# Optimization experiments

Hardware: AMD Instinct MI355X
Metric: run time of the kernel (lower is better)

Reference implementation:

```python
import jax, jax.numpy as jnp
import numpy as np

B_G = 16        # number of point clouds
N_PER = 32768   # points per cloud (equal -> no padding)
T = B_G * N_PER
CIN = 16
D = 32          # global_dim
H = 4           # num_heads
HD = D // H
L = 2           # layers
EPS_LN = 1e-5
EPS_Z = 1e-6


def setup_inputs() -> dict:
    key = jax.random.key(0)
    ks = jax.random.split(key, 32)
    r = lambda i, shape, s: (jax.random.normal(ks[i], shape, dtype=jnp.float32) * s)
    inp = {
        "x": r(0, (T, CIN), 1.0),
        "pos": r(1, (T, 3), 1.0),
        "batch": (jnp.arange(T, dtype=jnp.int32) // N_PER),
        "w_in": r(2, (CIN, D), CIN ** -0.5),
        "b_in": r(3, (D,), 0.02),
        "w_pos": r(4, (3, D), 3 ** -0.5),
        "b_pos": r(5, (D,), 0.02),
        "wq": r(6, (L, D, D), D ** -0.5),
        "bq": r(7, (L, D), 0.02),
        "wk": r(8, (L, D, D), D ** -0.5),
        "bk": r(9, (L, D), 0.02),
        "wv": r(10, (L, D, D), D ** -0.5),
        "bv": r(11, (L, D), 0.02),
        "wo": r(12, (L, D, D), D ** -0.5),
        "bo": r(13, (L, D), 0.02),
        "g1": jnp.ones((L, D), jnp.float32),
        "be1": jnp.zeros((L, D), jnp.float32),
        "w1": r(14, (L, D, 2 * D), D ** -0.5),
        "bf1": r(15, (L, 2 * D), 0.02),
        "w2": r(16, (L, 2 * D, D), (2 * D) ** -0.5),
        "bf2": r(17, (L, D), 0.02),
        "g2": jnp.ones((L, D), jnp.float32),
        "be2": jnp.zeros((L, D), jnp.float32),
    }
    return inp


def _layernorm(h, g, b):
    mu = jnp.mean(h, axis=-1, keepdims=True)
    var = jnp.mean(jnp.square(h - mu), axis=-1, keepdims=True)
    return (h - mu) * jax.lax.rsqrt(var + EPS_LN) * g + b


def _linear_attn(h, wq, bq, wk, bk, wv, bv, wo, bo):
    B, N, C = h.shape
    def heads(w, b):
        return (h @ w + b).reshape(B, N, H, HD).transpose(0, 2, 1, 3)  # [B,H,N,hd]
    q = jax.nn.elu(heads(wq, bq)) + 1.0   # ELU feature map phi(.)
    k = jax.nn.elu(heads(wk, bk)) + 1.0
    v = heads(wv, bv)
    kv = jnp.einsum("bhnd,bhne->bhde", k, v)            # O(N) KV summary
    ksum = k.sum(axis=2)                                   # [B,H,hd]
    z = 1.0 / (jnp.einsum("bhnd,bhd->bhn", q, ksum) + EPS_Z)
    out = jnp.einsum("bhnd,bhde->bhne", q, kv) * z[..., None]
    out = out.transpose(0, 2, 1, 3).reshape(B, N, C)
    return out @ wo + bo


def reference(x, pos, batch, w_in, b_in, w_pos, b_pos, wq, bq, wk, bk, wv, bv,
              wo, bo, g1, be1, w1, bf1, w2, bf2, g2, be2):
    # to_dense_batch: batch is sorted; compute per-point index within its segment
    counts = jax.ops.segment_sum(jnp.ones((T,), jnp.int32), batch, num_segments=B_G)
    starts = jnp.concatenate([jnp.zeros((1,), jnp.int32), jnp.cumsum(counts)[:-1]])
    idx = jnp.arange(T, dtype=jnp.int32) - starts[batch]
    x_dense = jnp.zeros((B_G, N_PER, CIN), x.dtype).at[batch, idx].set(x)
    pos_dense = jnp.zeros((B_G, N_PER, 3), pos.dtype).at[batch, idx].set(pos)

    h = (x_dense @ w_in + b_in) + (pos_dense @ w_pos + b_pos)  # [B,N,D]
    for l in range(L):
        h = _layernorm(h + _linear_attn(h, wq[l], bq[l], wk[l], bk[l],
                                        wv[l], bv[l], wo[l], bo[l]), g1[l], be1[l])
        ffn = jax.nn.relu(h @ w1[l] + bf1[l]) @ w2[l] + bf2[l]
        h = _layernorm(h + ffn, g2[l], be2[l])
    return h[batch, idx]  # back to [T, D] (h[mask])
```

## Files before the change

### kernel.cpp

```cpp
#include <hip/hip_runtime.h>

#define KVSZ 288
#define EPS_LN 1e-5f
#define EPS_Z  1e-6f

typedef __attribute__((ext_vector_type(8))) short bf16x8;
typedef __attribute__((ext_vector_type(4))) float f32x4;

#define MFMA(a, b, c) __builtin_amdgcn_mfma_f32_16x16x32_bf16(a, b, c, 0, 0, 0)

#define WQ  0
#define WO  1024
#define KVM 2048
#define W1  3072
#define W2  5120
#define WKN 7168
#define WVN 8192

__device__ __forceinline__ unsigned short f2bf(float f) {
  union { float f; unsigned u; } x; x.f = f;
  unsigned r = x.u + 0x7fff + ((x.u >> 16) & 1);
  return (unsigned short)(r >> 16);
}

__device__ __forceinline__ unsigned pkbf(float a, float b) {
#if __has_builtin(__builtin_amdgcn_cvt_pk_bf16_f32)
  typedef __attribute__((ext_vector_type(2))) __bf16 bf16x2_t;
  bf16x2_t v = __builtin_amdgcn_cvt_pk_bf16_f32(a, b);
  return __builtin_bit_cast(unsigned, v);
#else
  return (unsigned)f2bf(a) | ((unsigned)f2bf(b) << 16);
#endif
}

__device__ __forceinline__ void lds_fence() { asm volatile("s_waitcnt lgkmcnt(0)" ::: "memory"); }
__device__ __forceinline__ float phi(float x) { return x > 0.f ? x + 1.f : __expf(x); }

__device__ __forceinline__ int perm32(int kp) {
  return ((kp & 4) << 2) | (((kp >> 3) << 2) + (kp & 3));
}

__device__ __forceinline__ bf16x8 bbuild(f32x4 lo, f32x4 hi) {
  union { bf16x8 v; unsigned u[4]; } cv;
  cv.u[0] = pkbf(lo[0], lo[1]); cv.u[1] = pkbf(lo[2], lo[3]);
  cv.u[2] = pkbf(hi[0], hi[1]); cv.u[3] = pkbf(hi[2], hi[3]);
  return cv.v;
}

__device__ __forceinline__ void stage_a32(unsigned short* dst, const float* __restrict__ W,
                                          int N, int tid) {
  for (int i = tid; i < 32 * N; i += 256) {
    int n = i >> 5, kp = i & 31;
    dst[i] = f2bf(W[perm32(kp) * N + n]);
  }
}
__device__ __forceinline__ void stage_a64(unsigned short* dst, const float* __restrict__ W,
                                          int tid) {
  for (int i = tid; i < 64 * 32; i += 256) {
    int n = i >> 6, kp = i & 63;
    int kl = ((kp >> 5) << 5) + perm32(kp & 31);
    dst[i] = f2bf(W[kl * 32 + n]);
  }
}
__device__ __forceinline__ void stage_kvm_t(unsigned short* dst, const float* __restrict__ kvg,
                                            int tid) {
  for (int i = tid; i < 1024; i += 256) {
    int e = i >> 5, kp = i & 31;
    int d = perm32(kp);
    float v = ((d >> 3) == (e >> 3)) ? kvg[(e >> 3) * 64 + (d & 7) * 8 + (e & 7)] : 0.f;
    dst[i] = f2bf(v);
  }
}

__device__ __forceinline__ void ln_t(f32x4& a0, f32x4& a1, float4 g0, float4 g1,
                                     float4 b0, float4 b1) {
  float s = a0[0] + a0[1] + a0[2] + a0[3] + a1[0] + a1[1] + a1[2] + a1[3];
  s += __shfl_xor(s, 16); s += __shfl_xor(s, 32);
  float mu = s * (1.f / 32.f);
  float vv = 0.f;
#pragma unroll
  for (int r = 0; r < 4; r++) {
    a0[r] -= mu; a1[r] -= mu;
    vv += a0[r] * a0[r] + a1[r] * a1[r];
  }
  vv += __shfl_xor(vv, 16); vv += __shfl_xor(vv, 32);
  float rstd = rsqrtf(vv * (1.f / 32.f) + EPS_LN);
  a0[0] = a0[0] * rstd * g0.x + b0.x; a0[1] = a0[1] * rstd * g0.y + b0.y;
  a0[2] = a0[2] * rstd * g0.z + b0.z; a0[3] = a0[3] * rstd * g0.w + b0.w;
  a1[0] = a1[0] * rstd * g1.x + b1.x; a1[1] = a1[1] * rstd * g1.y + b1.y;
  a1[2] = a1[2] * rstd * g1.z + b1.z; a1[3] = a1[3] * rstd * g1.w + b1.w;
}

__device__ __forceinline__ void layer_core_t(
    f32x4* hc0, f32x4* hc1, const unsigned short* ws, int quad, int m,
    const float* __restrict__ bq, const float* __restrict__ bo,
    const float* __restrict__ g1, const float* __restrict__ be1,
    const float* __restrict__ bf1, const float* __restrict__ bf2,
    const float* __restrict__ g2, const float* __restrict__ be2,
    const float* __restrict__ kvg) {
  const int k0 = quad * 8, q4 = quad * 4;
  {
    const bf16x8 wqA0 = *(const bf16x8*)(ws + WQ + m * 32 + k0);
    const bf16x8 wqA1 = *(const bf16x8*)(ws + WQ + (16 + m) * 32 + k0);
    const bf16x8 kvA0 = *(const bf16x8*)(ws + KVM + m * 32 + k0);
    const bf16x8 kvA1 = *(const bf16x8*)(ws + KVM + (16 + m) * 32 + k0);
    const bf16x8 woA0 = *(const bf16x8*)(ws + WO + m * 32 + k0);
    const bf16x8 woA1 = *(const bf16x8*)(ws + WO + (16 + m) * 32 + k0);
    const float4 bq0 = *(const float4*)(bq + q4), bq1 = *(const float4*)(bq + 16 + q4);
    const float4 bo0 = *(const float4*)(bo + q4), bo1 = *(const float4*)(bo + 16 + q4);
    const float4 g10 = *(const float4*)(g1 + q4), g11 = *(const float4*)(g1 + 16 + q4);
    const float4 e10 = *(const float4*)(be1 + q4), e11 = *(const float4*)(be1 + 16 + q4);
    const float4 ks0 = *(const float4*)(kvg + 256 + q4);
    const float4 ks1 = *(const float4*)(kvg + 272 + q4);
#pragma unroll
    for (int mt = 0; mt < 4; mt++) {
      bf16x8 hB = bbuild(hc0[mt], hc1[mt]);
      f32x4 q0 = {bq0.x, bq0.y, bq0.z, bq0.w};
      f32x4 q1 = {bq1.x, bq1.y, bq1.z, bq1.w};
      q0 = MFMA(wqA0, hB, q0);
      q1 = MFMA(wqA1, hB, q1);
#pragma unroll
      for (int r = 0; r < 4; r++) { q0[r] = phi(q0[r]); q1[r] = phi(q1[r]); }
      bf16x8 qB = bbuild(q0, q1);
      f32x4 zz = {0.f, 0.f, 0.f, 0.f};
      f32x4 at0 = MFMA(kvA0, qB, zz);
      f32x4 at1 = MFMA(kvA1, qB, zz);
      float p0 = q0[0] * ks0.x + q0[1] * ks0.y + q0[2] * ks0.z + q0[3] * ks0.w;
      float p1 = q1[0] * ks1.x + q1[1] * ks1.y + q1[2] * ks1.z + q1[3] * ks1.w;
      p0 += __shfl_xor(p0, 16);
      p1 += __shfl_xor(p1, 16);
      float z0 = 1.f / (p0 + EPS_Z), z1 = 1.f / (p1 + EPS_Z);
      bf16x8 aB;
      {
        union { bf16x8 v; unsigned u[4]; } cv;
        cv.u[0] = pkbf(at0[0] * z0, at0[1] * z0); cv.u[1] = pkbf(at0[2] * z0, at0[3] * z0);
        cv.u[2] = pkbf(at1[0] * z1, at1[1] * z1); cv.u[3] = pkbf(at1[2] * z1, at1[3] * z1);
        aB = cv.v;
      }
      f32x4 h0 = hc0[mt], h1 = hc1[mt];
      h0[0] += bo0.x; h0[1] += bo0.y; h0[2] += bo0.z; h0[3] += bo0.w;
      h1[0] += bo1.x; h1[1] += bo1.y; h1[2] += bo1.z; h1[3] += bo1.w;
      h0 = MFMA(woA0, aB, h0);
      h1 = MFMA(woA1, aB, h1);
      ln_t(h0, h1, g10, g11, e10, e11);
      hc0[mt] = h0; hc1[mt] = h1;
    }
  }
  {
    bf16x8 w1A[4]; float4 b1f[4];
#pragma unroll
    for (int nt = 0; nt < 4; nt++) {
      w1A[nt] = *(const bf16x8*)(ws + W1 + (nt * 16 + m) * 32 + k0);
      b1f[nt] = *(const float4*)(bf1 + nt * 16 + q4);
    }
    const bf16x8 w2L0 = *(const bf16x8*)(ws + W2 + m * 64 + k0);
    const bf16x8 w2H0 = *(const bf16x8*)(ws + W2 + m * 64 + 32 + k0);
    const bf16x8 w2L1 = *(const bf16x8*)(ws + W2 + (16 + m) * 64 + k0);
    const bf16x8 w2H1 = *(const bf16x8*)(ws + W2 + (16 + m) * 64 + 32 + k0);
    const float4 b20 = *(const float4*)(bf2 + q4), b21 = *(const float4*)(bf2 + 16 + q4);
    const float4 g20 = *(const float4*)(g2 + q4), g21 = *(const float4*)(g2 + 16 + q4);
    const float4 e20 = *(const float4*)(be2 + q4), e21 = *(const float4*)(be2 + 16 + q4);
#pragma unroll
    for (int mt = 0; mt < 4; mt++) {
      bf16x8 hB = bbuild(hc0[mt], hc1[mt]);
      f32x4 hd[4];
#pragma unroll
      for (int nt = 0; nt < 4; nt++) {
        f32x4 ini = {b1f[nt].x, b1f[nt].y, b1f[nt].z, b1f[nt].w};
        hd[nt] = MFMA(w1A[nt], hB, ini);
#pragma unroll
        for (int r = 0; r < 4; r++) hd[nt][r] = fmaxf(hd[nt][r], 0.f);
      }
      bf16x8 fL = bbuild(hd[0], hd[1]);
      bf16x8 fH = bbuild(hd[2], hd[3]);
      f32x4 o0 = hc0[mt], o1 = hc1[mt];
      o0[0] += b20.x; o0[1] += b20.y; o0[2] += b20.z; o0[3] += b20.w;
      o1[0] += b21.x; o1[1] += b21.y; o1[2] += b21.z; o1[3] += b21.w;
      o0 = MFMA(w2L0, fL, o0);
      o0 = MFMA(w2H0, fH, o0);
      o1 = MFMA(w2L1, fL, o1);
      o1 = MFMA(w2H1, fH, o1);
      ln_t(o0, o1, g20, g21, e20, e21);
      hc0[mt] = o0; hc1[mt] = o1;
    }
  }
}

__device__ __forceinline__ void kv_stage_t(
    const f32x4* hc0, const f32x4* hc1, unsigned short* tw, const unsigned short* ws,
    int offk, int offv, float* blk, int quad, int m,
    const float* __restrict__ bk, const float* __restrict__ bv) {
  const int k0 = quad * 8, q4 = quad * 4;
  unsigned short* Tk = tw;
  unsigned short* Tv = tw + 1280;
  const bf16x8 wkA0 = *(const bf16x8*)(ws + offk + m * 32 + k0);
  const bf16x8 wkA1 = *(const bf16x8*)(ws + offk + (16 + m) * 32 + k0);
  const bf16x8 wvA0 = *(const bf16x8*)(ws + offv + m * 32 + k0);
  const bf16x8 wvA1 = *(const bf16x8*)(ws + offv + (16 + m) * 32 + k0);
  const float4 bk0 = *(const float4*)(bk + q4), bk1 = *(const float4*)(bk + 16 + q4);
  const float4 bv0 = *(const float4*)(bv + q4), bv1 = *(const float4*)(bv + 16 + q4);
  f32x4 accA = {0.f, 0.f, 0.f, 0.f}, accB = {0.f, 0.f, 0.f, 0.f};
  f32x4 ksa0 = {0.f, 0.f, 0.f, 0.f}, ksa1 = {0.f, 0.f, 0.f, 0.f};
#pragma unroll
  for (int ch = 0; ch < 2; ch++) {
#pragma unroll
    for (int mtl = 0; mtl < 2; mtl++) {
      int mt = ch * 2 + mtl;
      bf16x8 hB = bbuild(hc0[mt], hc1[mt]);
      f32x4 kn0 = {bk0.x, bk0.y, bk0.z, bk0.w};
      f32x4 kn1 = {bk1.x, bk1.y, bk1.z, bk1.w};
      f32x4 vn0 = {bv0.x, bv0.y, bv0.z, bv0.w};
      f32x4 vn1 = {bv1.x, bv1.y, bv1.z, bv1.w};
      kn0 = MFMA(wkA0, hB, kn0);
      kn1 = MFMA(wkA1, hB, kn1);
      vn0 = MFMA(wvA0, hB, vn0);
      vn1 = MFMA(wvA1, hB, vn1);
      int cb = mtl * 16 + m;
#pragma unroll
      for (int r = 0; r < 4; r++) {
        kn0[r] = phi(kn0[r]); kn1[r] = phi(kn1[r]);
        ksa0[r] += kn0[r];    ksa1[r] += kn1[r];
        Tk[(q4 + r) * 40 + cb]      = f2bf(kn0[r]);
        Tk[(16 + q4 + r) * 40 + cb] = f2bf(kn1[r]);
        Tv[(q4 + r) * 40 + cb]      = f2bf(vn0[r]);
        Tv[(16 + q4 + r) * 40 + cb] = f2bf(vn1[r]);
      }
    }
    lds_fence();
    bf16x8 akL = *(const bf16x8*)(Tk + m * 40 + k0);
    bf16x8 akH = *(const bf16x8*)(Tk + (16 + m) * 40 + k0);
    bf16x8 avL = *(const bf16x8*)(Tv + m * 40 + k0);
    bf16x8 avH = *(const bf16x8*)(Tv + (16 + m) * 40 + k0);
    accA = MFMA(akL, avL, accA);
    accB = MFMA(akH, avH, accB);
    lds_fence();
  }
#pragma unroll
  for (int r = 0; r < 4; r++) {
    float v0 = ksa0[r], v1 = ksa1[r];
    v0 += __shfl_xor(v0, 1); v0 += __shfl_xor(v0, 2); v0 += __shfl_xor(v0, 4); v0 += __shfl_xor(v0, 8);
    v1 += __shfl_xor(v1, 1); v1 += __shfl_xor(v1, 2); v1 += __shfl_xor(v1, 4); v1 += __shfl_xor(v1, 8);
    if (m == 0) {
      atomicAdd(&blk[256 + q4 + r], v0);
      atomicAdd(&blk[272 + q4 + r], v1);
    }
  }
  if ((quad >> 1) == (m >> 3)) {
    int h0 = quad >> 1, h1 = 2 + (quad >> 1), e = m & 7;
#pragma unroll
    for (int r = 0; r < 4; r++) {
      int d = (q4 + r) & 7;
      atomicAdd(&blk[h0 * 64 + d * 8 + e], accA[r]);
      atomicAdd(&blk[h1 * 64 + d * 8 + e], accB[r]);
    }
  }
}

__global__ __launch_bounds__(256) void k_embed(
    const float* __restrict__ x, const float* __restrict__ pos,
    const float* __restrict__ w_in, const float* __restrict__ b_in,
    const float* __restrict__ w_pos, const float* __restrict__ b_pos,
    const float* __restrict__ wk, const float* __restrict__ bk,
    const float* __restrict__ wv, const float* __restrict__ bv,
    float* __restrict__ hout, float* __restrict__ gkv) {
  __shared__ __align__(16) unsigned short ws[3072];
  __shared__ __align__(16) unsigned short tiles[4 * 2560];
  __shared__ float blk[KVSZ];
  const int tid = threadIdx.x;
  const int wv_ = tid >> 6, lane = tid & 63, quad = lane >> 4, m = lane & 15;
  unsigned short* tw = tiles + wv_ * 2560;
  for (int i = tid; i < 1024; i += 256) {
    int n = i >> 5, k = i & 31;
    float v = k < 16 ? w_in[k * 32 + n] : (k < 19 ? w_pos[(k - 16) * 32 + n] : 0.f);
    ws[i] = f2bf(v);
  }
  stage_a32(ws + 1024, wk, 32, tid);
  stage_a32(ws + 2048, wv, 32, tid);
  for (int i = tid; i < KVSZ; i += 256) blk[i] = 0.f;
  __syncthreads();
  const int wbase = blockIdx.x * 256 + wv_ * 64;
  const int cloud = blockIdx.x >> 7;
  const int k0 = quad * 8, q4 = quad * 4;
  const bf16x8 weA0 = *(const bf16x8*)(ws + m * 32 + k0);
  const bf16x8 weA1 = *(const bf16x8*)(ws + (16 + m) * 32 + k0);
  float4 bi0, bi1;
  {
    float4 a = *(const float4*)(b_in + q4), b = *(const float4*)(b_pos + q4);
    bi0 = make_float4(a.x + b.x, a.y + b.y, a.z + b.z, a.w + b.w);
    float4 c = *(const float4*)(b_in + 16 + q4), d = *(const float4*)(b_pos + 16 + q4);
    bi1 = make_float4(c.x + d.x, c.y + d.y, c.z + d.z, c.w + d.w);
  }
  f32x4 hc0[4], hc1[4];
#pragma unroll
  for (int mt = 0; mt < 4; mt++) {
    int p = wbase + mt * 16 + m;
    union { bf16x8 v; unsigned u[4]; } xb;
    xb.u[0] = xb.u[1] = xb.u[2] = xb.u[3] = 0;
    if (quad < 2) {
      const float4* xp = (const float4*)(x + (size_t)p * 16 + quad * 8);
      float4 t0 = xp[0], t1 = xp[1];
      xb.u[0] = pkbf(t0.x, t0.y); xb.u[1] = pkbf(t0.z, t0.w);
      xb.u[2] = pkbf(t1.x, t1.y); xb.u[3] = pkbf(t1.z, t1.w);
    } else if (quad == 2) {
      const float* pp = pos + (size_t)p * 3;
      xb.u[0] = pkbf(pp[0], pp[1]); xb.u[1] = pkbf(pp[2], 0.f);
    }
    f32x4 i0 = {bi0.x, bi0.y, bi0.z, bi0.w};
    f32x4 i1 = {bi1.x, bi1.y, bi1.z, bi1.w};
    hc0[mt] = MFMA(weA0, xb.v, i0);
    hc1[mt] = MFMA(weA1, xb.v, i1);
    float* hp = hout + (size_t)p * 32;
    *(float4*)(hp + q4)      = make_float4(hc0[mt][0], hc0[mt][1], hc0[mt][2], hc0[mt][3]);
    *(float4*)(hp + 16 + q4) = make_float4(hc1[mt][0], hc1[mt][1], hc1[mt][2], hc1[mt][3]);
  }
  kv_stage_t(hc0, hc1, tw, ws, 1024, 2048, blk, quad, m, bk, bv);
  __syncthreads();
  float* g = gkv + cloud * KVSZ;
  for (int i = tid; i < KVSZ; i += 256) atomicAdd(&g[i], blk[i]);
}

__global__ __launch_bounds__(256) void k_mid(
    const float* __restrict__ wq, const float* __restrict__ bq,
    const float* __restrict__ wo, const float* __restrict__ bo,
    const float* __restrict__ g1, const float* __restrict__ be1,
    const float* __restrict__ w1, const float* __restrict__ bf1,
    const float* __restrict__ w2, const float* __restrict__ bf2,
    const float* __restrict__ g2, const float* __restrict__ be2,
    const float* __restrict__ wkn, const float* __restrict__ bkn,
    const float* __restrict__ wvn, const float* __restrict__ bvn,
    const float* __restrict__ kv_in, float* __restrict__ gkv_out,
    float* __restrict__ hbuf) {
  __shared__ __align__(16) unsigned short ws[9216];
  __shared__ __align__(16) unsigned short tiles[4 * 2560];
  __shared__ float blk[KVSZ];
  const int tid = threadIdx.x;
  const int wv_ = tid >> 6, lane = tid & 63, quad = lane >> 4, m = lane & 15;
  unsigned short* tw = tiles + wv_ * 2560;
  const int cloud = blockIdx.x >> 7;
  stage_a32(ws + WQ, wq, 32, tid);
  stage_a32(ws + WO, wo, 32, tid);
  stage_kvm_t(ws + KVM, kv_in + cloud * KVSZ, tid);
  stage_a32(ws + W1, w1, 64, tid);
  stage_a64(ws + W2, w2, tid);
  stage_a32(ws + WKN, wkn, 32, tid);
  stage_a32(ws + WVN, wvn, 32, tid);
  for (int i = tid; i < KVSZ; i += 256) blk[i] = 0.f;
  __syncthreads();
  const int wbase = blockIdx.x * 256 + wv_ * 64;
  const int q4 = quad * 4;
  f32x4 hc0[4], hc1[4];
#pragma unroll
  for (int mt = 0; mt < 4; mt++) {
    const float* hp = hbuf + (size_t)(wbase + mt * 16 + m) * 32;
    float4 lo = *(const float4*)(hp + q4);
    float4 hi = *(const float4*)(hp + 16 + q4);
    hc0[mt][0] = lo.x; hc0[mt][1] = lo.y; hc0[mt][2] = lo.z; hc0[mt][3] = lo.w;
    hc1[mt][0] = hi.x; hc1[mt][1] = hi.y; hc1[mt][2] = hi.z; hc1[mt][3] = hi.w;
  }
  layer_core_t(hc0, hc1, ws, quad, m, bq, bo, g1, be1, bf1, bf2, g2, be2,
               kv_in + cloud * KVSZ);
#pragma unroll
  for (int mt = 0; mt < 4; mt++) {
    float* hp = hbuf + (size_t)(wbase + mt * 16 + m) * 32;
    *(float4*)(hp + q4)      = make_float4(hc0[mt][0], hc0[mt][1], hc0[mt][2], hc0[mt][3]);
    *(float4*)(hp + 16 + q4) = make_float4(hc1[mt][0], hc1[mt][1], hc1[mt][2], hc1[mt][3]);
  }
  kv_stage_t(hc0, hc1, tw, ws, WKN, WVN, blk, quad, m, bkn, bvn);
  __syncthreads();
  float* g = gkv_out + cloud * KVSZ;
  for (int i = tid; i < KVSZ; i += 256) atomicAdd(&g[i], blk[i]);
}

__global__ __launch_bounds__(256) void k_last(
    const float* __restrict__ wq, const float* __restrict__ bq,
    const float* __restrict__ wo, const float* __restrict__ bo,
    const float* __restrict__ g1, const float* __restrict__ be1,
    const float* __restrict__ w1, const float* __restrict__ bf1,
    const float* __restrict__ w2, const float* __restrict__ bf2,
    const float* __restrict__ g2, const float* __restrict__ be2,
    const float* __restrict__ kv_in, float* __restrict__ hbuf) {
  __shared__ __align__(16) unsigned short ws[7168];
  const int tid = threadIdx.x;
  const int wv_ = tid >> 6, lane = tid & 63, quad = lane >> 4, m = lane & 15;
  const int cloud = blockIdx.x >> 7;
  stage_a32(ws + WQ, wq, 32, tid);
  stage_a32(ws + WO, wo, 32, tid);
  stage_kvm_t(ws + KVM, kv_in + cloud * KVSZ, tid);
  stage_a32(ws + W1, w1, 64, tid);
  stage_a64(ws + W2, w2, tid);
  __syncthreads();
  const int wbase = blockIdx.x * 256 + wv_ * 64;
  const int q4 = quad * 4;
  f32x4 hc0[4], hc1[4];
#pragma unroll
  for (int mt = 0; mt < 4; mt++) {
    const float* hp = hbuf + (size_t)(wbase + mt * 16 + m) * 32;
    float4 lo = *(const float4*)(hp + q4);
    float4 hi = *(const float4*)(hp + 16 + q4);
    hc0[mt][0] = lo.x; hc0[mt][1] = lo.y; hc0[mt][2] = lo.z; hc0[mt][3] = lo.w;
    hc1[mt][0] = hi.x; hc1[mt][1] = hi.y; hc1[mt][2] = hi.z; hc1[mt][3] = hi.w;
  }
  layer_core_t(hc0, hc1, ws, quad, m, bq, bo, g1, be1, bf1, bf2, g2, be2,
               kv_in + cloud * KVSZ);
#pragma unroll
  for (int mt = 0; mt < 4; mt++) {
    float* hp = hbuf + (size_t)(wbase + mt * 16 + m) * 32;
    *(float4*)(hp + q4)      = make_float4(hc0[mt][0], hc0[mt][1], hc0[mt][2], hc0[mt][3]);
    *(float4*)(hp + 16 + q4) = make_float4(hc1[mt][0], hc1[mt][1], hc1[mt][2], hc1[mt][3]);
  }
}

extern "C" void kernel_launch(void* const* d_in, const int* in_sizes, int n_in,
                              void* d_out, int out_size, void* d_ws, size_t ws_size,
                              hipStream_t stream) {
  (void)in_sizes; (void)n_in; (void)out_size; (void)ws_size;
  const float* x     = (const float*)d_in[0];
  const float* pos   = (const float*)d_in[1];
  const float* w_in  = (const float*)d_in[3];
  const float* b_in  = (const float*)d_in[4];
  const float* w_pos = (const float*)d_in[5];
  const float* b_pos = (const float*)d_in[6];
  const float* wq  = (const float*)d_in[7];
  const float* bq  = (const float*)d_in[8];
  const float* wk  = (const float*)d_in[9];
  const float* bk  = (const float*)d_in[10];
  const float* wv  = (const float*)d_in[11];
  const float* bv  = (const float*)d_in[12];
  const float* wo  = (const float*)d_in[13];
  const float* bo  = (const float*)d_in[14];
  const float* g1  = (const float*)d_in[15];
  const float* be1 = (const float*)d_in[16];
  const float* w1  = (const float*)d_in[17];
  const float* bf1 = (const float*)d_in[18];
  const float* w2  = (const float*)d_in[19];
  const float* bf2 = (const float*)d_in[20];
  const float* g2  = (const float*)d_in[21];
  const float* be2 = (const float*)d_in[22];
  float* out   = (float*)d_out;
  float* kvbuf = (float*)d_ws;

  hipMemsetAsync(kvbuf, 0, 2 * 16 * KVSZ * sizeof(float), stream);
  dim3 grid(2048), block(256);
  k_embed<<<grid, block, 0, stream>>>(x, pos, w_in, b_in, w_pos, b_pos,
                                      wk, bk, wv, bv, out, kvbuf);
  k_mid<<<grid, block, 0, stream>>>(wq, bq, wo, bo, g1, be1, w1, bf1, w2, bf2, g2, be2,
                                    wk + 1024, bk + 32, wv + 1024, bv + 32,
                                    kvbuf, kvbuf + 16 * KVSZ, out);
  k_last<<<grid, block, 0, stream>>>(wq + 1024, bq + 32, wo + 1024, bo + 32,
                                     g1 + 32, be1 + 32, w1 + 2048, bf1 + 64,
                                     w2 + 2048, bf2 + 32, g2 + 32, be2 + 32,
                                     kvbuf + 16 * KVSZ, out);
}
```

Baseline: 306.9 us.

## Fuse three layer kernels into one persistent kernel with grid barriers

```diff
diff --git a/kernel.cpp b/kernel.cpp
--- a/kernel.cpp
+++ b/kernel.cpp
@@ -3,6 +3,7 @@
 #define KVSZ 288
 #define EPS_LN 1e-5f
 #define EPS_Z  1e-6f
+#define NBLK 512
 
 typedef __attribute__((ext_vector_type(8))) short bf16x8;
 typedef __attribute__((ext_vector_type(4))) float f32x4;
@@ -36,6 +37,20 @@
 __device__ __forceinline__ void lds_fence() { asm volatile("s_waitcnt lgkmcnt(0)" ::: "memory"); }
 __device__ __forceinline__ float phi(float x) { return x > 0.f ? x + 1.f : __expf(x); }
 
+__device__ __forceinline__ float gread_rmw(const float* p) {
+  return atomicAdd((float*)p, 0.0f);
+}
+
+__device__ __forceinline__ void grid_barrier(unsigned* ctr) {
+  __syncthreads();
+  if (threadIdx.x == 0) {
+    __threadfence();
+    atomicAdd(ctr, 1u);
+    while (atomicAdd(ctr, 0u) < NBLK) __builtin_amdgcn_s_sleep(2);
+  }
+  __syncthreads();
+}
+
 __device__ __forceinline__ int perm32(int kp) {
   return ((kp & 4) << 2) | (((kp >> 3) << 2) + (kp & 3));
 }
@@ -67,7 +82,7 @@
   for (int i = tid; i < 1024; i += 256) {
     int e = i >> 5, kp = i & 31;
     int d = perm32(kp);
-    float v = ((d >> 3) == (e >> 3)) ? kvg[(e >> 3) * 64 + (d & 7) * 8 + (e & 7)] : 0.f;
+    float v = ((d >> 3) == (e >> 3)) ? gread_rmw(&kvg[(e >> 3) * 64 + (d & 7) * 8 + (e & 7)]) : 0.f;
     dst[i] = f2bf(v);
   }
 }
@@ -92,12 +107,12 @@
 }
 
 __device__ __forceinline__ void layer_core_t(
-    f32x4* hc0, f32x4* hc1, const unsigned short* ws, int quad, int m,
+    f32x4* hc0, f32x4* hc1, const unsigned short* ws, const float* kss,
+    int quad, int m,
     const float* __restrict__ bq, const float* __restrict__ bo,
     const float* __restrict__ g1, const float* __restrict__ be1,
     const float* __restrict__ bf1, const float* __restrict__ bf2,
-    const float* __restrict__ g2, const float* __restrict__ be2,
-    const float* __restrict__ kvg) {
+    const float* __restrict__ g2, const float* __restrict__ be2) {
   const int k0 = quad * 8, q4 = quad * 4;
   {
     const bf16x8 wqA0 = *(const bf16x8*)(ws + WQ + m * 32 + k0);
@@ -110,8 +125,8 @@
     const float4 bo0 = *(const float4*)(bo + q4), bo1 = *(const float4*)(bo + 16 + q4);
     const float4 g10 = *(const float4*)(g1 + q4), g11 = *(const float4*)(g1 + 16 + q4);
     const float4 e10 = *(const float4*)(be1 + q4), e11 = *(const float4*)(be1 + 16 + q4);
-    const float4 ks0 = *(const float4*)(kvg + 256 + q4);
-    const float4 ks1 = *(const float4*)(kvg + 272 + q4);
+    const float4 ks0 = *(const float4*)(kss + q4);
+    const float4 ks1 = *(const float4*)(kss + 16 + q4);
 #pragma unroll
     for (int mt = 0; mt < 4; mt++) {
       bf16x8 hB = bbuild(hc0[mt], hc1[mt]);
@@ -256,155 +271,121 @@
   }
 }
 
-__global__ __launch_bounds__(256) void k_embed(
+__global__ __launch_bounds__(256, 2) void k_fused(
     const float* __restrict__ x, const float* __restrict__ pos,
     const float* __restrict__ w_in, const float* __restrict__ b_in,
     const float* __restrict__ w_pos, const float* __restrict__ b_pos,
+    const float* __restrict__ wq, const float* __restrict__ bq,
     const float* __restrict__ wk, const float* __restrict__ bk,
     const float* __restrict__ wv, const float* __restrict__ bv,
-    float* __restrict__ hout, float* __restrict__ gkv) {
-  __shared__ __align__(16) unsigned short ws[3072];
-  __shared__ __align__(16) unsigned short tiles[4 * 2560];
-  __shared__ float blk[KVSZ];
-  const int tid = threadIdx.x;
-  const int wv_ = tid >> 6, lane = tid & 63, quad = lane >> 4, m = lane & 15;
-  unsigned short* tw = tiles + wv_ * 2560;
-  for (int i = tid; i < 1024; i += 256) {
-    int n = i >> 5, k = i & 31;
-    float v = k < 16 ? w_in[k * 32 + n] : (k < 19 ? w_pos[(k - 16) * 32 + n] : 0.f);
-    ws[i] = f2bf(v);
-  }
-  stage_a32(ws + 1024, wk, 32, tid);
-  stage_a32(ws + 2048, wv, 32, tid);
-  for (int i = tid; i < KVSZ; i += 256) blk[i] = 0.f;
-  __syncthreads();
-  const int wbase = blockIdx.x * 256 + wv_ * 64;
-  const int cloud = blockIdx.x >> 7;
-  const int k0 = quad * 8, q4 = quad * 4;
-  const bf16x8 weA0 = *(const bf16x8*)(ws + m * 32 + k0);
-  const bf16x8 weA1 = *(const bf16x8*)(ws + (16 + m) * 32 + k0);
-  float4 bi0, bi1;
-  {
-    float4 a = *(const float4*)(b_in + q4), b = *(const float4*)(b_pos + q4);
-    bi0 = make_float4(a.x + b.x, a.y + b.y, a.z + b.z, a.w + b.w);
-    float4 c = *(const float4*)(b_in + 16 + q4), d = *(const float4*)(b_pos + 16 + q4);
-    bi1 = make_float4(c.x + d.x, c.y + d.y, c.z + d.z, c.w + d.w);
-  }
-  f32x4 hc0[4], hc1[4];
-#pragma unroll
-  for (int mt = 0; mt < 4; mt++) {
-    int p = wbase + mt * 16 + m;
-    union { bf16x8 v; unsigned u[4]; } xb;
-    xb.u[0] = xb.u[1] = xb.u[2] = xb.u[3] = 0;
-    if (quad < 2) {
-      const float4* xp = (const float4*)(x + (size_t)p * 16 + quad * 8);
-      float4 t0 = xp[0], t1 = xp[1];
-      xb.u[0] = pkbf(t0.x, t0.y); xb.u[1] = pkbf(t0.z, t0.w);
-      xb.u[2] = pkbf(t1.x, t1.y); xb.u[3] = pkbf(t1.z, t1.w);
-    } else if (quad == 2) {
-      const float* pp = pos + (size_t)p * 3;
-      xb.u[0] = pkbf(pp[0], pp[1]); xb.u[1] = pkbf(pp[2], 0.f);
-    }
-    f32x4 i0 = {bi0.x, bi0.y, bi0.z, bi0.w};
-    f32x4 i1 = {bi1.x, bi1.y, bi1.z, bi1.w};
-    hc0[mt] = MFMA(weA0, xb.v, i0);
-    hc1[mt] = MFMA(weA1, xb.v, i1);
-    float* hp = hout + (size_t)p * 32;
-    *(float4*)(hp + q4)      = make_float4(hc0[mt][0], hc0[mt][1], hc0[mt][2], hc0[mt][3]);
-    *(float4*)(hp + 16 + q4) = make_float4(hc1[mt][0], hc1[mt][1], hc1[mt][2], hc1[mt][3]);
-  }
-  kv_stage_t(hc0, hc1, tw, ws, 1024, 2048, blk, quad, m, bk, bv);
-  __syncthreads();
-  float* g = gkv + cloud * KVSZ;
-  for (int i = tid; i < KVSZ; i += 256) atomicAdd(&g[i], blk[i]);
-}
-
-__global__ __launch_bounds__(256) void k_mid(
-    const float* __restrict__ wq, const float* __restrict__ bq,
     const float* __restrict__ wo, const float* __restrict__ bo,
     const float* __restrict__ g1, const float* __restrict__ be1,
     const float* __restrict__ w1, const float* __restrict__ bf1,
     const float* __restrict__ w2, const float* __restrict__ bf2,
     const float* __restrict__ g2, const float* __restrict__ be2,
-    const float* __restrict__ wkn, const float* __restrict__ bkn,
-    const float* __restrict__ wvn, const float* __restrict__ bvn,
-    const float* __restrict__ kv_in, float* __restrict__ gkv_out,
-    float* __restrict__ hbuf) {
+    float* __restrict__ out, float* __restrict__ kvbuf) {
   __shared__ __align__(16) unsigned short ws[9216];
   __shared__ __align__(16) unsigned short tiles[4 * 2560];
   __shared__ float blk[KVSZ];
+  __shared__ float kss[32];
   const int tid = threadIdx.x;
   const int wv_ = tid >> 6, lane = tid & 63, quad = lane >> 4, m = lane & 15;
   unsigned short* tw = tiles + wv_ * 2560;
-  const int cloud = blockIdx.x >> 7;
+  const int cloud = blockIdx.x >> 5;
+  float* gkv0 = kvbuf + cloud * KVSZ;
+  float* gkv1 = kvbuf + (16 + cloud) * KVSZ;
+  unsigned* ctrs = (unsigned*)(kvbuf + 2 * 16 * KVSZ);
+  const int wbase = blockIdx.x * 1024 + wv_ * 256;
+  const int k0 = quad * 8, q4 = quad * 4;
+
+  for (int i = tid; i < 1024; i += 256) {
+    int n = i >> 5, k = i & 31;
+    float v = k < 16 ? w_in[k * 32 + n] : (k < 19 ? w_pos[(k - 16) * 32 + n] : 0.f);
+    ws[i] = f2bf(v);
+  }
+  stage_a32(ws + 1024, wk, 32, tid);
+  stage_a32(ws + 2048, wv, 32, tid);
+  for (int i = tid; i < KVSZ; i += 256) blk[i] = 0.f;
+  __syncthreads();
+
+  f32x4 hc0[16], hc1[16];
+  {
+    const bf16x8 weA0 = *(const bf16x8*)(ws + m * 32 + k0);
+    const bf16x8 weA1 = *(const bf16x8*)(ws + (16 + m) * 32 + k0);
+    float4 bi0, bi1;
+    {
+      float4 a = *(const float4*)(b_in + q4), b = *(const float4*)(b_pos + q4);
+      bi0 = make_float4(a.x + b.x, a.y + b.y, a.z + b.z, a.w + b.w);
+      float4 c = *(const float4*)(b_in + 16 + q4), d = *(const float4*)(b_pos + 16 + q4);
+      bi1 = make_float4(c.x + d.x, c.y + d.y, c.z + d.z, c.w + d.w);
+    }
+#pragma unroll
+    for (int mt = 0; mt < 16; mt++) {
+      int p = wbase + mt * 16 + m;
+      union { bf16x8 v; unsigned u[4]; } xb;
+      xb.u[0] = xb.u[1] = xb.u[2] = xb.u[3] = 0;
+      if (quad < 2) {
+        const float4* xp = (const float4*)(x + (size_t)p * 16 + quad * 8);
+        float4 t0 = xp[0], t1 = xp[1];
+        xb.u[0] = pkbf(t0.x, t0.y); xb.u[1] = pkbf(t0.z, t0.w);
+        xb.u[2] = pkbf(t1.x, t1.y); xb.u[3] = pkbf(t1.z, t1.w);
+      } else if (quad == 2) {
+        const float* pp = pos + (size_t)p * 3;
+        xb.u[0] = pkbf(pp[0], pp[1]); xb.u[1] = pkbf(pp[2], 0.f);
+      }
+      f32x4 i0 = {bi0.x, bi0.y, bi0.z, bi0.w};
+      f32x4 i1 = {bi1.x, bi1.y, bi1.z, bi1.w};
+      hc0[mt] = MFMA(weA0, xb.v, i0);
+      hc1[mt] = MFMA(weA1, xb.v, i1);
+    }
+  }
+#pragma unroll
+  for (int hh = 0; hh < 4; hh++)
+    kv_stage_t(hc0 + hh * 4, hc1 + hh * 4, tw, ws, 1024, 2048, blk, quad, m, bk, bv);
+  __syncthreads();
+  for (int i = tid; i < KVSZ; i += 256) atomicAdd(&gkv0[i], blk[i]);
+  grid_barrier(&ctrs[0]);
+
   stage_a32(ws + WQ, wq, 32, tid);
   stage_a32(ws + WO, wo, 32, tid);
-  stage_kvm_t(ws + KVM, kv_in + cloud * KVSZ, tid);
+  stage_kvm_t(ws + KVM, gkv0, tid);
   stage_a32(ws + W1, w1, 64, tid);
   stage_a64(ws + W2, w2, tid);
-  stage_a32(ws + WKN, wkn, 32, tid);
-  stage_a32(ws + WVN, wvn, 32, tid);
+  stage_a32(ws + WKN, wk + 1024, 32, tid);
+  stage_a32(ws + WVN, wv + 1024, 32, tid);
+  if (tid < 32) kss[tid] = gread_rmw(gkv0 + 256 + tid);
   for (int i = tid; i < KVSZ; i += 256) blk[i] = 0.f;
   __syncthreads();
-  const int wbase = blockIdx.x * 256 + wv_ * 64;
-  const int q4 = quad * 4;
-  f32x4 hc0[4], hc1[4];
-#pragma unroll
-  for (int mt = 0; mt < 4; mt++) {
-    const float* hp = hbuf + (size_t)(wbase + mt * 16 + m) * 32;
-    float4 lo = *(const float4*)(hp + q4);
-    float4 hi = *(const float4*)(hp + 16 + q4);
-    hc0[mt][0] = lo.x; hc0[mt][1] = lo.y; hc0[mt][2] = lo.z; hc0[mt][3] = lo.w;
-    hc1[mt][0] = hi.x; hc1[mt][1] = hi.y; hc1[mt][2] = hi.z; hc1[mt][3] = hi.w;
-  }
-  layer_core_t(hc0, hc1, ws, quad, m, bq, bo, g1, be1, bf1, bf2, g2, be2,
-               kv_in + cloud * KVSZ);
-#pragma unroll
-  for (int mt = 0; mt < 4; mt++) {
-    float* hp = hbuf + (size_t)(wbase + mt * 16 + m) * 32;
-    *(float4*)(hp + q4)      = make_float4(hc0[mt][0], hc0[mt][1], hc0[mt][2], hc0[mt][3]);
-    *(float4*)(hp + 16 + q4) = make_float4(hc1[mt][0], hc1[mt][1], hc1[mt][2], hc1[mt][3]);
-  }
-  kv_stage_t(hc0, hc1, tw, ws, WKN, WVN, blk, quad, m, bkn, bvn);
-  __syncthreads();
-  float* g = gkv_out + cloud * KVSZ;
-  for (int i = tid; i < KVSZ; i += 256) atomicAdd(&g[i], blk[i]);
-}
-
-__global__ __launch_bounds__(256) void k_last(
-    const float* __restrict__ wq, const float* __restrict__ bq,
-    const float* __restrict__ wo, const float* __restrict__ bo,
-    const float* __restrict__ g1, const float* __restrict__ be1,
-    const float* __restrict__ w1, const float* __restrict__ bf1,
-    const float* __restrict__ w2, const float* __restrict__ bf2,
-    const float* __restrict__ g2, const float* __restrict__ be2,
-    const float* __restrict__ kv_in, float* __restrict__ hbuf) {
-  __shared__ __align__(16) unsigned short ws[7168];
-  const int tid = threadIdx.x;
-  const int wv_ = tid >> 6, lane = tid & 63, quad = lane >> 4, m = lane & 15;
-  const int cloud = blockIdx.x >> 7;
-  stage_a32(ws + WQ, wq, 32, tid);
-  stage_a32(ws + WO, wo, 32, tid);
-  stage_kvm_t(ws + KVM, kv_in + cloud * KVSZ, tid);
-  stage_a32(ws + W1, w1, 64, tid);
-  stage_a64(ws + W2, w2, tid);
-  __syncthreads();
-  const int wbase = blockIdx.x * 256 + wv_ * 64;
-  const int q4 = quad * 4;
-  f32x4 hc0[4], hc1[4];
-#pragma unroll
-  for (int mt = 0; mt < 4; mt++) {
-    const float* hp = hbuf + (size_t)(wbase + mt * 16 + m) * 32;
-    float4 lo = *(const float4*)(hp + q4);
-    float4 hi = *(const float4*)(hp + 16 + q4);
-    hc0[mt][0] = lo.x; hc0[mt][1] = lo.y; hc0[mt][2] = lo.z; hc0[mt][3] = lo.w;
-    hc1[mt][0] = hi.x; hc1[mt][1] = hi.y; hc1[mt][2] = hi.z; hc1[mt][3] = hi.w;
-  }
-  layer_core_t(hc0, hc1, ws, quad, m, bq, bo, g1, be1, bf1, bf2, g2, be2,
-               kv_in + cloud * KVSZ);
-#pragma unroll
-  for (int mt = 0; mt < 4; mt++) {
-    float* hp = hbuf + (size_t)(wbase + mt * 16 + m) * 32;
+
+#pragma unroll
+  for (int hh = 0; hh < 4; hh++)
+    layer_core_t(hc0 + hh * 4, hc1 + hh * 4, ws, kss, quad, m,
+                 bq, bo, g1, be1, bf1, bf2, g2, be2);
+#pragma unroll
+  for (int hh = 0; hh < 4; hh++)
+    kv_stage_t(hc0 + hh * 4, hc1 + hh * 4, tw, ws, WKN, WVN, blk, quad, m,
+               bk + 32, bv + 32);
+  __syncthreads();
+  for (int i = tid; i < KVSZ; i += 256) atomicAdd(&gkv1[i], blk[i]);
+  grid_barrier(&ctrs[1]);
+
+  stage_a32(ws + WQ, wq + 1024, 32, tid);
+  stage_a32(ws + WO, wo + 1024, 32, tid);
+  stage_kvm_t(ws + KVM, gkv1, tid);
+  stage_a32(ws + W1, w1 + 2048, 64, tid);
+  stage_a64(ws + W2, w2 + 2048, tid);
+  if (tid < 32) kss[tid] = gread_rmw(gkv1 + 256 + tid);
+  __syncthreads();
+
+#pragma unroll
+  for (int hh = 0; hh < 4; hh++)
+    layer_core_t(hc0 + hh * 4, hc1 + hh * 4, ws, kss, quad, m,
+                 bq + 32, bo + 32, g1 + 32, be1 + 32, bf1 + 64, bf2 + 32,
+                 g2 + 32, be2 + 32);
+#pragma unroll
+  for (int mt = 0; mt < 16; mt++) {
+    int p = wbase + mt * 16 + m;
+    float* hp = out + (size_t)p * 32;
     *(float4*)(hp + q4)      = make_float4(hc0[mt][0], hc0[mt][1], hc0[mt][2], hc0[mt][3]);
     *(float4*)(hp + 16 + q4) = make_float4(hc1[mt][0], hc1[mt][1], hc1[mt][2], hc1[mt][3]);
   }
@@ -439,15 +420,8 @@
   float* out   = (float*)d_out;
   float* kvbuf = (float*)d_ws;
 
-  hipMemsetAsync(kvbuf, 0, 2 * 16 * KVSZ * sizeof(float), stream);
-  dim3 grid(2048), block(256);
-  k_embed<<<grid, block, 0, stream>>>(x, pos, w_in, b_in, w_pos, b_pos,
-                                      wk, bk, wv, bv, out, kvbuf);
-  k_mid<<<grid, block, 0, stream>>>(wq, bq, wo, bo, g1, be1, w1, bf1, w2, bf2, g2, be2,
-                                    wk + 1024, bk + 32, wv + 1024, bv + 32,
-                                    kvbuf, kvbuf + 16 * KVSZ, out);
-  k_last<<<grid, block, 0, stream>>>(wq + 1024, bq + 32, wo + 1024, bo + 32,
-                                     g1 + 32, be1 + 32, w1 + 2048, bf1 + 64,
-                                     w2 + 2048, bf2 + 32, g2 + 32, be2 + 32,
-                                     kvbuf + 16 * KVSZ, out);
-}
+  hipMemsetAsync(kvbuf, 0, 2 * 16 * KVSZ * sizeof(float) + 64, stream);
+  k_fused<<<dim3(NBLK), dim3(256), 0, stream>>>(
+      x, pos, w_in, b_in, w_pos, b_pos, wq, bq, wk, bk, wv, bv, wo, bo,
+      g1, be1, w1, bf1, w2, bf2, g2, be2, out, kvbuf);
+}
```

Result: slower. 416.4 us (+35.7%).
